# Kernel tuning notes

Measured on AMD Instinct MI355X. Metric: run time of the kernel, lower is better.

The kernel has to match this reference:

```python
import jax, jax.numpy as jnp
import numpy as np

B, S, HID = 4, 2048, 576
NH, NKV, HD = 9, 3, 64
MAXPOS, THETA = 8192, 100000.0


def rotate_half(x):
    x1, x2 = x[..., : x.shape[-1] // 2], x[..., x.shape[-1] // 2 :]
    return jnp.concatenate((-x2, x1), axis=-1)


def setup_inputs() -> dict:
    key = jax.random.key(0)
    ks = jax.random.split(key, 6)
    x = jax.random.normal(ks[0], (B, S, HID), dtype=jnp.float32)
    # RoPE tables (HuggingFace layout: freqs duplicated across halves)
    inv_freq = 1.0 / (THETA ** (np.arange(0, HD, 2, dtype=np.float32) / HD))
    freqs = np.outer(np.arange(MAXPOS, dtype=np.float32), inv_freq)
    emb = np.concatenate([freqs, freqs], axis=-1)
    cos = jnp.asarray(np.cos(emb))
    sin = jnp.asarray(np.sin(emb))
    position_ids = jnp.broadcast_to(jnp.arange(S, dtype=jnp.int64), (B, S))
    # additive causal mask [B,1,S,S]
    causal = jnp.where(
        jnp.tril(jnp.ones((S, S), dtype=bool)), 0.0, -1e9
    ).astype(jnp.float32)
    attention_mask = jnp.broadcast_to(causal, (B, 1, S, S))
    scale = 0.02
    wq = jax.random.normal(ks[1], (NH * HD, HID), dtype=jnp.float32) * scale
    wk = jax.random.normal(ks[2], (NKV * HD, HID), dtype=jnp.float32) * scale
    wv = jax.random.normal(ks[3], (NKV * HD, HID), dtype=jnp.float32) * scale
    wo = jax.random.normal(ks[4], (HID, NH * HD), dtype=jnp.float32) * scale
    return {
        "x": x, "cos": cos, "sin": sin, "position_ids": position_ids,
        "attention_mask": attention_mask,
        "wq": wq, "wk": wk, "wv": wv, "wo": wo,
    }


def reference(x, cos, sin, position_ids, attention_mask, wq, wk, wv, wo):
    b, s, _ = x.shape
    # projections (nn.Linear: y = x @ W.T), split into heads -> [B,H,S,D]
    q = (x @ wq.T).reshape(b, s, NH, HD).transpose(0, 2, 1, 3)
    k = (x @ wk.T).reshape(b, s, NKV, HD).transpose(0, 2, 1, 3)
    v = (x @ wv.T).reshape(b, s, NKV, HD).transpose(0, 2, 1, 3)
    # RoPE: cos/sin gathered per position -> [B,1,S,D], broadcast over heads
    c = cos[position_ids][:, None, :, :]
    si = sin[position_ids][:, None, :, :]
    q = q * c + rotate_half(q) * si
    k = k * c + rotate_half(k) * si
    # GQA expansion: repeat_interleave kv heads to match q heads
    k = jnp.repeat(k, NH // NKV, axis=1)
    v = jnp.repeat(v, NH // NKV, axis=1)
    scale = 1.0 / jnp.sqrt(jnp.asarray(HD, dtype=x.dtype))
    scores = jnp.einsum("bhqd,bhkd->bhqk", q, k) * scale + attention_mask
    attn = jax.nn.softmax(scores.astype(jnp.float32), axis=-1).astype(q.dtype)
    out = jnp.einsum("bhqk,bhkd->bhqd", attn, v)
    out = out.transpose(0, 2, 1, 3).reshape(b, s, NH * HD)
    return out @ wo.T
```

## Files before the change

### kernel.cpp

```cpp
#include <hip/hip_runtime.h>
#include <hip/hip_bf16.h>

#define B_    4
#define S_    2048
#define HID_  576
#define NH_   9
#define NKV_  3
#define HD_   64
#define GQ_   3

typedef __attribute__((ext_vector_type(8))) short bf16x8;
typedef __attribute__((ext_vector_type(4))) float f32x4;
typedef __attribute__((ext_vector_type(16))) float f32x16;

__device__ __forceinline__ short f2bf(float f) {
    union { float f; unsigned int u; } v; v.f = f;
    unsigned int r = (v.u + 0x7fffu + ((v.u >> 16) & 1u)) >> 16;
    return (short)r;
}

__device__ __forceinline__ unsigned int cvt_pk_bf16(float a, float b) {
    unsigned int r;
    asm("v_cvt_pk_bf16_f32 %0, %1, %2" : "=v"(r) : "v"(a), "v"(b));
    return r;
}

__device__ __forceinline__ float exp2fast(float x) {
    return __builtin_amdgcn_exp2f(x);
}

__device__ __forceinline__ void async16(const void* g, void* l) {
    __builtin_amdgcn_global_load_lds(
        (const __attribute__((address_space(1))) unsigned int*)g,
        (__attribute__((address_space(3))) unsigned int*)l, 16, 0, 0);
}

#define NX_   (8192 * 576)
#define NWQ_  (576 * 576)
#define NWK_  (192 * 576)
#define NWV_  (192 * 576)
#define NWO_  (576 * 576)
#define NTOT_ (NX_ + NWQ_ + NWK_ + NWV_ + NWO_)

__global__ __launch_bounds__(256) void convert_kernel(
    const float* __restrict__ x,  const float* __restrict__ wq,
    const float* __restrict__ wk, const float* __restrict__ wv,
    const float* __restrict__ wo,
    short* __restrict__ xb, short* __restrict__ wqkvb, short* __restrict__ wob)
{
    int i4 = (blockIdx.x * 256 + threadIdx.x) * 4;
    const float* src; short* dst;
    if (i4 < NX_)                          { src = x  + i4;                          dst = xb    + i4; }
    else if (i4 < NX_ + NWQ_)              { src = wq + (i4 - NX_);                  dst = wqkvb + (i4 - NX_); }
    else if (i4 < NX_ + NWQ_ + NWK_)       { src = wk + (i4 - NX_ - NWQ_);           dst = wqkvb + (i4 - NX_); }
    else if (i4 < NX_ + NWQ_ + NWK_ + NWV_){ src = wv + (i4 - NX_ - NWQ_ - NWK_);    dst = wqkvb + (i4 - NX_); }
    else                                   { src = wo + (i4 - NX_ - NWQ_ - NWK_ - NWV_);
                                             dst = wob + (i4 - NX_ - NWQ_ - NWK_ - NWV_); }
    float4 v = *(const float4*)src;
    short4 o = make_short4(f2bf(v.x), f2bf(v.y), f2bf(v.z), f2bf(v.w));
    *(short4*)dst = o;
}

__global__ __launch_bounds__(256) void qkv_kernel(
    const short* __restrict__ xb,
    const short* __restrict__ wqkvb,
    const float* __restrict__ cosb,
    const float* __restrict__ sinb,
    short* __restrict__ Q,
    short* __restrict__ K,
    short* __restrict__ Vt)
{
    __shared__ __align__(16) short As[2][256 * 64];
    __shared__ __align__(16) short Bs[2][64 * 64];

    const int bid = blockIdx.x;
    const int f   = (bid & 7) * 60 + (bid >> 3);
    const int m0     = (f / 15) * 256;
    const int nb_blk = f % 15;
    const int tid  = threadIdx.x;
    const int w    = tid >> 6, lane = tid & 63;
    const int quad = lane >> 4, c = lane & 15;
    const int lr   = lane >> 3, lg = lane & 7;
    const int sw   = lg ^ lr;
    const int xg   = quad ^ (c & 7);

    auto stage = [&](int step, short* dstA, short* dstB) {
        const int k0 = step * 64;
        #pragma unroll
        for (int r = 0; r < 8; ++r) {
            int ch = w * 8 + r, R = ch * 8 + lr;
            async16(xb + (size_t)(m0 + R) * HID_ + k0 + sw * 8, (char*)dstA + ch * 1024);
        }
        #pragma unroll
        for (int r = 0; r < 2; ++r) {
            int ch = w * 2 + r, R = ch * 8 + lr;
            async16(wqkvb + (size_t)(nb_blk * 64 + R) * HID_ + k0 + sw * 8, (char*)dstB + ch * 1024);
        }
    };

    f32x4 acc[4][4];
    #pragma unroll
    for (int mt = 0; mt < 4; ++mt)
        #pragma unroll
        for (int nb = 0; nb < 4; ++nb) acc[mt][nb] = (f32x4){0.f, 0.f, 0.f, 0.f};

    stage(0, As[0], Bs[0]);

    int buf = 0;
    for (int kk = 0; kk < 9; ++kk) {
        __syncthreads();
        if (kk < 8) stage(kk + 1, As[buf ^ 1], Bs[buf ^ 1]);

        const short* a_s = As[buf];
        const short* b_s = Bs[buf];
        bf16x8 bfr[4][2];
        #pragma unroll
        for (int nb = 0; nb < 4; ++nb) {
            int row = nb * 16 + c;
            bfr[nb][0] = *(const bf16x8*)(b_s + row * 64 + xg * 8);
            bfr[nb][1] = *(const bf16x8*)(b_s + row * 64 + (xg ^ 4) * 8);
        }
        #pragma unroll
        for (int mt = 0; mt < 4; ++mt) {
            int row = w * 64 + mt * 16 + c;
            bf16x8 a0 = *(const bf16x8*)(a_s + row * 64 + xg * 8);
            bf16x8 a1 = *(const bf16x8*)(a_s + row * 64 + (xg ^ 4) * 8);
            #pragma unroll
            for (int nb = 0; nb < 4; ++nb) {
                acc[mt][nb] = __builtin_amdgcn_mfma_f32_16x16x32_bf16(a0, bfr[nb][0], acc[mt][nb], 0, 0, 0);
                acc[mt][nb] = __builtin_amdgcn_mfma_f32_16x16x32_bf16(a1, bfr[nb][1], acc[mt][nb], 0, 0, 0);
            }
        }
        buf ^= 1;
    }

    int type, head;
    if (nb_blk < NH_)            { type = 0; head = nb_blk; }
    else if (nb_blk < NH_ + NKV_){ type = 1; head = nb_blk - NH_; }
    else                         { type = 2; head = nb_blk - NH_ - NKV_; }
    const int b  = m0 >> 11;
    const int s0 = m0 & (S_ - 1);

    if (type < 2) {
        const float qs = (type == 0) ? 0.18033688f : 1.0f;
        #pragma unroll
        for (int mt = 0; mt < 4; ++mt)
            #pragma unroll
            for (int reg = 0; reg < 4; ++reg) {
                int s = s0 + w * 64 + mt * 16 + quad * 4 + reg;
                const float* cr = cosb + (size_t)s * HD_;
                const float* sr = sinb + (size_t)s * HD_;
                float a0 = acc[mt][0][reg], a1 = acc[mt][1][reg];
                float a2 = acc[mt][2][reg], a3 = acc[mt][3][reg];
                float o0 = (a0 * cr[c]      - a2 * sr[c])      * qs;
                float o1 = (a1 * cr[c + 16] - a3 * sr[c + 16]) * qs;
                float o2 = (a2 * cr[c + 32] + a0 * sr[c + 32]) * qs;
                float o3 = (a3 * cr[c + 48] + a1 * sr[c + 48]) * qs;
                short* dst = (type == 0)
                    ? Q + (((size_t)b * NH_  + head) * S_ + s) * HD_
                    : K + (((size_t)b * NKV_ + head) * S_ + s) * HD_;
                dst[c]      = f2bf(o0);
                dst[c + 16] = f2bf(o1);
                dst[c + 32] = f2bf(o2);
                dst[c + 48] = f2bf(o3);
            }
    } else {
        short* base = Vt + (((size_t)b * NKV_ + head) * HD_) * S_;
        #pragma unroll
        for (int mt = 0; mt < 4; ++mt) {
            int s4 = s0 + w * 64 + mt * 16 + quad * 4;
            #pragma unroll
            for (int nb = 0; nb < 4; ++nb) {
                int d = nb * 16 + c;
                short4 pk = make_short4(f2bf(acc[mt][nb][0]), f2bf(acc[mt][nb][1]),
                                        f2bf(acc[mt][nb][2]), f2bf(acc[mt][nb][3]));
                *(short4*)(base + (size_t)d * S_ + s4) = pk;
            }
        }
    }
}

#define CPAD 528

__global__ __launch_bounds__(256) void attn_kernel(
    const short* __restrict__ Q,
    const short* __restrict__ K,
    const short* __restrict__ Vt,
    short* __restrict__ AOb)
{
    __shared__ __align__(16) char smem[33792];

    const int hb = blockIdx.x;
    const int h  = hb >> 2, b = hb & 3;
    const int qt = 31 - blockIdx.y;
    const int kh = h / GQ_;
    const int tid  = threadIdx.x;
    const int w    = tid >> 6, lane = tid & 63;
    const int l31  = lane & 31, hi = lane >> 5, l7 = lane & 7;
    const int lr   = lane >> 3, lg = lane & 7;
    const int sw   = lg ^ lr;
    const int qh   = w >> 1, kv = w & 1;
    const int rb   = (l31 >> 3) * CPAD + l7 * 64;

    const short* Qg = Q  + (((size_t)b * NH_  + h ) * S_ + qt * 64) * HD_;
    const short* Kg = K  + (((size_t)b * NKV_ + kh) * S_) * HD_;
    const short* Vg = Vt + (((size_t)b * NKV_ + kh) * HD_) * S_;

    bf16x8 aq[4];
    #pragma unroll
    for (int ks = 0; ks < 4; ++ks)
        aq[ks] = *(const bf16x8*)(Qg + (size_t)(qh * 32 + l31) * HD_ + (2 * ks + hi) * 8);

    const bool stK = (w < 2);
    const int  ch0 = (w & 1) * 4;
    const short* gs[4];
    #pragma unroll
    for (int r = 0; r < 4; ++r) {
        int ch = ch0 + r;
        gs[r] = stK ? Kg + (size_t)(ch * 8 + lr) * HD_ + sw * 8
                    : Vg + (size_t)(ch * 8 + lr) * S_  + sw * 8;
    }
    const int gstep = stK ? 64 * HD_ : 64;
    char* lbase = smem + (stK ? 0 : 16896);

    #pragma unroll
    for (int r = 0; r < 4; ++r)
        async16(gs[r], lbase + (ch0 + r) * 1056);

    f32x16 acc_o[2];
    #pragma unroll
    for (int dt = 0; dt < 2; ++dt)
        #pragma unroll
        for (int i = 0; i < 16; ++i) acc_o[dt][i] = 0.f;
    float acc_ls = 0.f;

    auto do_tile = [&](int buf, bool MASK) {
        if (MASK && kv > qh) return;
        const short* ksb = (const short*)(smem + buf * 8448);
        const short* vsb = (const short*)(smem + 16896 + buf * 8448);
        f32x16 z;
        #pragma unroll
        for (int i = 0; i < 16; ++i) z[i] = -4.0f;
        #pragma unroll
        for (int ks = 0; ks < 4; ++ks) {
            bf16x8 ak = *(const bf16x8*)(ksb + kv * 4 * CPAD + rb + ((2 * ks + hi) ^ l7) * 8);
            z = __builtin_amdgcn_mfma_f32_32x32x16_bf16(ak, aq[ks], z, 0, 0, 0);
        }
        float p[16];
        #pragma unroll
        for (int r = 0; r < 16; ++r) {
            float pv = exp2fast(z[r]);
            if (MASK && kv == qh && ((r & 3) + 8 * (r >> 2) + 4 * hi > l31)) pv = 0.f;
            p[r] = pv;
        }
        float lp = 0.f;
        #pragma unroll
        for (int r = 0; r < 16; ++r) lp += p[r];
        acc_ls += lp;
        #pragma unroll
        for (int k2 = 0; k2 < 2; ++k2) {
            unsigned int u0 = cvt_pk_bf16(p[k2 * 8 + 0], p[k2 * 8 + 1]);
            unsigned int u1 = cvt_pk_bf16(p[k2 * 8 + 2], p[k2 * 8 + 3]);
            unsigned int v0 = cvt_pk_bf16(p[k2 * 8 + 4], p[k2 * 8 + 5]);
            unsigned int v1 = cvt_pk_bf16(p[k2 * 8 + 6], p[k2 * 8 + 7]);
            asm("v_permlane32_swap_b32 %0, %1" : "+v"(u0), "+v"(v0));
            asm("v_permlane32_swap_b32 %0, %1" : "+v"(u1), "+v"(v1));
            union { unsigned int u[4]; bf16x8 v8; } af;
            af.u[0] = u0; af.u[1] = u1; af.u[2] = v0; af.u[3] = v1;
            #pragma unroll
            for (int dt = 0; dt < 2; ++dt) {
                bf16x8 bv = *(const bf16x8*)(vsb + dt * 4 * CPAD + rb + ((kv * 4 + k2 * 2 + hi) ^ l7) * 8);
                acc_o[dt] = __builtin_amdgcn_mfma_f32_32x32x16_bf16(af.v8, bv, acc_o[dt], 0, 0, 0);
            }
        }
    };

    __syncthreads();
    int buf = 0;
    for (int kt = 0; kt < qt; ++kt) {
        #pragma unroll
        for (int r = 0; r < 4; ++r) {
            gs[r] += gstep;
            async16(gs[r], lbase + (buf ^ 1) * 8448 + (ch0 + r) * 1056);
        }
        do_tile(buf, false);
        __syncthreads();
        buf ^= 1;
    }
    do_tile(buf, true);

    float ls2 = acc_ls + __shfl_xor(acc_ls, 32);
    float* sc  = (float*)smem;
    float* scl = (float*)(smem + 16384);
    __syncthreads();
    if (kv == 1) {
        #pragma unroll
        for (int dt = 0; dt < 2; ++dt)
            #pragma unroll
            for (int r = 0; r < 16; ++r)
                sc[qh * 2048 + (dt * 16 + r) * 64 + lane] = acc_o[dt][r];
        if (lane < 32) scl[qh * 32 + lane] = ls2;
    }
    __syncthreads();
    if (kv == 0) {
        #pragma unroll
        for (int dt = 0; dt < 2; ++dt)
            #pragma unroll
            for (int r = 0; r < 16; ++r)
                acc_o[dt][r] += sc[qh * 2048 + (dt * 16 + r) * 64 + lane];
        float lt = ls2 + scl[qh * 32 + l31];
        float linv = 1.0f / lt;
        if (lane < 32) scl[qh * 32 + lane] = linv;
        #pragma unroll
        for (int dt = 0; dt < 2; ++dt)
            #pragma unroll
            for (int r = 0; r < 16; ++r) {
                int q = (r & 3) + 8 * (r >> 2) + 4 * hi;
                int s = qt * 64 + qh * 32 + q;
                float li = scl[qh * 32 + q];
                AOb[(((size_t)b * S_ + s) * NH_ + h) * HD_ + dt * 32 + l31] =
                    f2bf(acc_o[dt][r] * li);
            }
    }
}

__global__ __launch_bounds__(256) void oproj_kernel(
    const short* __restrict__ AOb,
    const short* __restrict__ wob,
    float* __restrict__ out)
{
    __shared__ __align__(16) short As[2][256 * 64];
    __shared__ __align__(16) short Bs[2][64 * 64];

    const int bid = blockIdx.x;
    const int f   = (bid & 7) * 36 + (bid >> 3);
    const int m0 = (f / 9) * 256;
    const int n0 = (f % 9) * 64;
    const int tid  = threadIdx.x;
    const int w    = tid >> 6, lane = tid & 63;
    const int quad = lane >> 4, c = lane & 15;
    const int lr   = lane >> 3, lg = lane & 7;
    const int sw   = lg ^ lr;
    const int xg   = quad ^ (c & 7);

    auto stage = [&](int step, short* dstA, short* dstB) {
        const int k0 = step * 64;
        #pragma unroll
        for (int r = 0; r < 8; ++r) {
            int ch = w * 8 + r, R = ch * 8 + lr;
            async16(AOb + (size_t)(m0 + R) * HID_ + k0 + sw * 8, (char*)dstA + ch * 1024);
        }
        #pragma unroll
        for (int r = 0; r < 2; ++r) {
            int ch = w * 2 + r, R = ch * 8 + lr;
            async16(wob + (size_t)(n0 + R) * HID_ + k0 + sw * 8, (char*)dstB + ch * 1024);
        }
    };

    f32x4 acc[4][4];
    #pragma unroll
    for (int mt = 0; mt < 4; ++mt)
        #pragma unroll
        for (int nb = 0; nb < 4; ++nb) acc[mt][nb] = (f32x4){0.f, 0.f, 0.f, 0.f};

    stage(0, As[0], Bs[0]);

    int buf = 0;
    for (int kk = 0; kk < 9; ++kk) {
        __syncthreads();
        if (kk < 8) stage(kk + 1, As[buf ^ 1], Bs[buf ^ 1]);

        const short* a_s = As[buf];
        const short* b_s = Bs[buf];
        bf16x8 bfr[4][2];
        #pragma unroll
        for (int nb = 0; nb < 4; ++nb) {
            int row = nb * 16 + c;
            bfr[nb][0] = *(const bf16x8*)(b_s + row * 64 + xg * 8);
            bfr[nb][1] = *(const bf16x8*)(b_s + row * 64 + (xg ^ 4) * 8);
        }
        #pragma unroll
        for (int mt = 0; mt < 4; ++mt) {
            int row = w * 64 + mt * 16 + c;
            bf16x8 a0 = *(const bf16x8*)(a_s + row * 64 + xg * 8);
            bf16x8 a1 = *(const bf16x8*)(a_s + row * 64 + (xg ^ 4) * 8);
            #pragma unroll
            for (int nb = 0; nb < 4; ++nb) {
                acc[mt][nb] = __builtin_amdgcn_mfma_f32_16x16x32_bf16(a0, bfr[nb][0], acc[mt][nb], 0, 0, 0);
                acc[mt][nb] = __builtin_amdgcn_mfma_f32_16x16x32_bf16(a1, bfr[nb][1], acc[mt][nb], 0, 0, 0);
            }
        }
        buf ^= 1;
    }

    #pragma unroll
    for (int mt = 0; mt < 4; ++mt)
        #pragma unroll
        for (int reg = 0; reg < 4; ++reg) {
            int m = m0 + w * 64 + mt * 16 + quad * 4 + reg;
            float* dst = out + (size_t)m * HID_ + n0;
            #pragma unroll
            for (int nb = 0; nb < 4; ++nb)
                dst[nb * 16 + c] = acc[mt][nb][reg];
        }
}

extern "C" void kernel_launch(void* const* d_in, const int* in_sizes, int n_in,
                              void* d_out, int out_size, void* d_ws, size_t ws_size,
                              hipStream_t stream) {
    const float* x    = (const float*)d_in[0];
    const float* cosb = (const float*)d_in[1];
    const float* sinb = (const float*)d_in[2];
    const float* wq   = (const float*)d_in[5];
    const float* wk   = (const float*)d_in[6];
    const float* wv   = (const float*)d_in[7];
    const float* wo   = (const float*)d_in[8];

    short* xb    = (short*)d_ws;
    short* wqkvb = xb    + (size_t)NX_;
    short* wob   = wqkvb + (size_t)(NWQ_ + NWK_ + NWV_);
    short* Qb    = wob   + (size_t)NWO_;
    short* Kb    = Qb    + (size_t)B_ * NH_  * S_ * HD_;
    short* Vtb   = Kb    + (size_t)B_ * NKV_ * S_ * HD_;
    short* AOb   = Vtb   + (size_t)B_ * NKV_ * S_ * HD_;

    convert_kernel<<<dim3(NTOT_ / 4 / 256), dim3(256), 0, stream>>>(
        x, wq, wk, wv, wo, xb, wqkvb, wob);
    qkv_kernel<<<dim3(480), dim3(256), 0, stream>>>(
        xb, wqkvb, cosb, sinb, Qb, Kb, Vtb);
    attn_kernel<<<dim3(36, 32), dim3(256), 0, stream>>>(Qb, Kb, Vtb, AOb);
    oproj_kernel<<<dim3(288), dim3(256), 0, stream>>>(AOb, wob, (float*)d_out);
}
```

Before: 186.3 us.

## Triple-buffer K/V tiles in attention with two-deep async prefetch

Replaces the double-buffered K/V staging loop with a three-buffer ring that prefetches two tiles ahead, using explicit vmcnt waits and raw s_barrier instead of __syncthreads. The aim is to hide more global-load latency behind the MFMA work of the current tile. It raises shared memory per block from about 33KB to about 50KB, which may reduce the number of resident blocks per CU, and relies on hand-counted vmcnt values being correct.

```diff
diff --git a/kernel.cpp b/kernel.cpp
--- a/kernel.cpp
+++ b/kernel.cpp
@@ -181,6 +181,7 @@
 }
 
 #define CPAD 528
+#define TILEB 8448
 
 __global__ __launch_bounds__(256) void attn_kernel(
     const short* __restrict__ Q,
@@ -188,7 +189,7 @@
     const short* __restrict__ Vt,
     short* __restrict__ AOb)
 {
-    __shared__ __align__(16) char smem[33792];
+    __shared__ __align__(16) char smem[50688];
 
     const int hb = blockIdx.x;
     const int h  = hb >> 2, b = hb & 3;
@@ -213,19 +214,19 @@
 
     const bool stK = (w < 2);
     const int  ch0 = (w & 1) * 4;
-    const short* gs[4];
-    #pragma unroll
-    for (int r = 0; r < 4; ++r) {
-        int ch = ch0 + r;
-        gs[r] = stK ? Kg + (size_t)(ch * 8 + lr) * HD_ + sw * 8
-                    : Vg + (size_t)(ch * 8 + lr) * S_  + sw * 8;
-    }
-    const int gstep = stK ? 64 * HD_ : 64;
-    char* lbase = smem + (stK ? 0 : 16896);
-
-    #pragma unroll
-    for (int r = 0; r < 4; ++r)
-        async16(gs[r], lbase + (ch0 + r) * 1056);
+    const int  doff = stK ? 0 : TILEB;
+
+    auto stagebuf = [&](int kt, int ib) {
+        char* dst = smem + ib * (2 * TILEB) + doff;
+        #pragma unroll
+        for (int r = 0; r < 4; ++r) {
+            int ch = ch0 + r;
+            const short* src = stK
+                ? Kg + (size_t)(kt * 64 + ch * 8 + lr) * HD_ + sw * 8
+                : Vg + (size_t)(ch * 8 + lr) * S_ + kt * 64 + sw * 8;
+            async16(src, dst + ch * 1056);
+        }
+    };
 
     f32x16 acc_o[2];
     #pragma unroll
@@ -234,10 +235,10 @@
         for (int i = 0; i < 16; ++i) acc_o[dt][i] = 0.f;
     float acc_ls = 0.f;
 
-    auto do_tile = [&](int buf, bool MASK) {
+    auto do_tile = [&](int ib, bool MASK) {
         if (MASK && kv > qh) return;
-        const short* ksb = (const short*)(smem + buf * 8448);
-        const short* vsb = (const short*)(smem + 16896 + buf * 8448);
+        const short* ksb = (const short*)(smem + ib * (2 * TILEB));
+        const short* vsb = (const short*)(smem + ib * (2 * TILEB) + TILEB);
         f32x16 z;
         #pragma unroll
         for (int i = 0; i < 16; ++i) z[i] = -4.0f;
@@ -275,19 +276,27 @@
         }
     };
 
-    __syncthreads();
-    int buf = 0;
-    for (int kt = 0; kt < qt; ++kt) {
-        #pragma unroll
-        for (int r = 0; r < 4; ++r) {
-            gs[r] += gstep;
-            async16(gs[r], lbase + (buf ^ 1) * 8448 + (ch0 + r) * 1056);
-        }
-        do_tile(buf, false);
-        __syncthreads();
-        buf ^= 1;
-    }
-    do_tile(buf, true);
+    stagebuf(0, 0);
+    stagebuf(qt > 0 ? 1 : 0, 1);
+    asm volatile("s_waitcnt vmcnt(4)" ::: "memory");
+    __builtin_amdgcn_sched_barrier(0);
+    __builtin_amdgcn_s_barrier();
+
+    int cur = 0, pre = 2;
+    for (int kt = 0; kt <= qt; ++kt) {
+        const bool more = (kt + 2 <= qt);
+        if (more) stagebuf(kt + 2, pre);
+        do_tile(cur, kt == qt);
+        if (more) {
+            asm volatile("s_waitcnt vmcnt(4)" ::: "memory");
+        } else {
+            asm volatile("s_waitcnt vmcnt(0)" ::: "memory");
+        }
+        __builtin_amdgcn_sched_barrier(0);
+        __builtin_amdgcn_s_barrier();
+        cur = (cur == 2) ? 0 : cur + 1;
+        pre = (pre == 2) ? 0 : pre + 1;
+    }
 
     float ls2 = acc_ls + __shfl_xor(acc_ls, 32);
     float* sc  = (float*)smem;
```

After: 196.6 us. 1.05x slower.

## Compute softmax row sums via MFMA with ones vector and drop LDS padding

Applied to the files above, without the earlier changes.

Replaces the per-lane scalar accumulation of softmax probabilities with an extra MFMA that multiplies the bf16 probability fragment by a vector of ones, so row sums land in the same layout as the output accumulator. It also removes the padded shared-memory row stride in favour of an unpadded XOR-swizzled layout, shrinking LDS use. The intent is to cut VALU add work in the inner loop and simplify addressing. The trade-off is an extra matrix instruction per k-chunk, sums computed from bf16-rounded probabilities, and a possible change in bank conflicts with the new layout.

```diff
diff --git a/kernel.cpp b/kernel.cpp
--- a/kernel.cpp
+++ b/kernel.cpp
@@ -180,15 +180,13 @@
     }
 }
 
-#define CPAD 528
-
 __global__ __launch_bounds__(256) void attn_kernel(
     const short* __restrict__ Q,
     const short* __restrict__ K,
     const short* __restrict__ Vt,
     short* __restrict__ AOb)
 {
-    __shared__ __align__(16) char smem[33792];
+    __shared__ __align__(16) char smem[32768];
 
     const int hb = blockIdx.x;
     const int h  = hb >> 2, b = hb & 3;
@@ -200,7 +198,6 @@
     const int lr   = lane >> 3, lg = lane & 7;
     const int sw   = lg ^ lr;
     const int qh   = w >> 1, kv = w & 1;
-    const int rb   = (l31 >> 3) * CPAD + l7 * 64;
 
     const short* Qg = Q  + (((size_t)b * NH_  + h ) * S_ + qt * 64) * HD_;
     const short* Kg = K  + (((size_t)b * NKV_ + kh) * S_) * HD_;
@@ -213,6 +210,7 @@
 
     const bool stK = (w < 2);
     const int  ch0 = (w & 1) * 4;
+    const int  doff = stK ? 0 : 16384;
     const short* gs[4];
     #pragma unroll
     for (int r = 0; r < 4; ++r) {
@@ -221,29 +219,39 @@
                     : Vg + (size_t)(ch * 8 + lr) * S_  + sw * 8;
     }
     const int gstep = stK ? 64 * HD_ : 64;
-    char* lbase = smem + (stK ? 0 : 16896);
-
-    #pragma unroll
-    for (int r = 0; r < 4; ++r)
-        async16(gs[r], lbase + (ch0 + r) * 1056);
+
+    auto stagebuf = [&](int ib) {
+        char* dst = smem + doff + ib * 8192;
+        #pragma unroll
+        for (int r = 0; r < 4; ++r) {
+            async16(gs[r], dst + (ch0 + r) * 1024);
+            gs[r] += gstep;
+        }
+    };
+
+    bf16x8 ones;
+    #pragma unroll
+    for (int i = 0; i < 8; ++i) ones[i] = (short)0x3F80;
 
     f32x16 acc_o[2];
     #pragma unroll
     for (int dt = 0; dt < 2; ++dt)
         #pragma unroll
         for (int i = 0; i < 16; ++i) acc_o[dt][i] = 0.f;
-    float acc_ls = 0.f;
-
-    auto do_tile = [&](int buf, bool MASK) {
+    f32x16 acc_l;
+    #pragma unroll
+    for (int i = 0; i < 16; ++i) acc_l[i] = 0.f;
+
+    auto do_tile = [&](int ib, bool MASK) {
         if (MASK && kv > qh) return;
-        const short* ksb = (const short*)(smem + buf * 8448);
-        const short* vsb = (const short*)(smem + 16896 + buf * 8448);
+        const short* ksb = (const short*)(smem + ib * 8192);
+        const short* vsb = (const short*)(smem + 16384 + ib * 8192);
         f32x16 z;
         #pragma unroll
         for (int i = 0; i < 16; ++i) z[i] = -4.0f;
         #pragma unroll
         for (int ks = 0; ks < 4; ++ks) {
-            bf16x8 ak = *(const bf16x8*)(ksb + kv * 4 * CPAD + rb + ((2 * ks + hi) ^ l7) * 8);
+            bf16x8 ak = *(const bf16x8*)(ksb + (kv * 32 + l31) * 64 + ((2 * ks + hi) ^ l7) * 8);
             z = __builtin_amdgcn_mfma_f32_32x32x16_bf16(ak, aq[ks], z, 0, 0, 0);
         }
         float p[16];
@@ -253,10 +261,6 @@
             if (MASK && kv == qh && ((r & 3) + 8 * (r >> 2) + 4 * hi > l31)) pv = 0.f;
             p[r] = pv;
         }
-        float lp = 0.f;
-        #pragma unroll
-        for (int r = 0; r < 16; ++r) lp += p[r];
-        acc_ls += lp;
         #pragma unroll
         for (int k2 = 0; k2 < 2; ++k2) {
             unsigned int u0 = cvt_pk_bf16(p[k2 * 8 + 0], p[k2 * 8 + 1]);
@@ -269,27 +273,24 @@
             af.u[0] = u0; af.u[1] = u1; af.u[2] = v0; af.u[3] = v1;
             #pragma unroll
             for (int dt = 0; dt < 2; ++dt) {
-                bf16x8 bv = *(const bf16x8*)(vsb + dt * 4 * CPAD + rb + ((kv * 4 + k2 * 2 + hi) ^ l7) * 8);
+                bf16x8 bv = *(const bf16x8*)(vsb + (dt * 32 + l31) * 64 + ((kv * 4 + k2 * 2 + hi) ^ l7) * 8);
                 acc_o[dt] = __builtin_amdgcn_mfma_f32_32x32x16_bf16(af.v8, bv, acc_o[dt], 0, 0, 0);
             }
+            acc_l = __builtin_amdgcn_mfma_f32_32x32x16_bf16(af.v8, ones, acc_l, 0, 0, 0);
         }
     };
 
+    stagebuf(0);
     __syncthreads();
     int buf = 0;
     for (int kt = 0; kt < qt; ++kt) {
-        #pragma unroll
-        for (int r = 0; r < 4; ++r) {
-            gs[r] += gstep;
-            async16(gs[r], lbase + (buf ^ 1) * 8448 + (ch0 + r) * 1056);
-        }
+        stagebuf(buf ^ 1);
         do_tile(buf, false);
         __syncthreads();
         buf ^= 1;
     }
     do_tile(buf, true);
 
-    float ls2 = acc_ls + __shfl_xor(acc_ls, 32);
     float* sc  = (float*)smem;
     float* scl = (float*)(smem + 16384);
     __syncthreads();
@@ -299,27 +300,29 @@
             #pragma unroll
             for (int r = 0; r < 16; ++r)
                 sc[qh * 2048 + (dt * 16 + r) * 64 + lane] = acc_o[dt][r];
-        if (lane < 32) scl[qh * 32 + lane] = ls2;
+        if (l31 == 0) {
+            #pragma unroll
+            for (int r = 0; r < 16; ++r)
+                scl[qh * 32 + (r & 3) + 8 * (r >> 2) + 4 * hi] = acc_l[r];
+        }
     }
     __syncthreads();
     if (kv == 0) {
+        float linv[16];
+        #pragma unroll
+        for (int r = 0; r < 16; ++r) {
+            int q = (r & 3) + 8 * (r >> 2) + 4 * hi;
+            linv[r] = 1.0f / (acc_l[r] + scl[qh * 32 + q]);
+        }
         #pragma unroll
         for (int dt = 0; dt < 2; ++dt)
             #pragma unroll
-            for (int r = 0; r < 16; ++r)
-                acc_o[dt][r] += sc[qh * 2048 + (dt * 16 + r) * 64 + lane];
-        float lt = ls2 + scl[qh * 32 + l31];
-        float linv = 1.0f / lt;
-        if (lane < 32) scl[qh * 32 + lane] = linv;
-        #pragma unroll
-        for (int dt = 0; dt < 2; ++dt)
-            #pragma unroll
             for (int r = 0; r < 16; ++r) {
+                float o = acc_o[dt][r] + sc[qh * 2048 + (dt * 16 + r) * 64 + lane];
                 int q = (r & 3) + 8 * (r >> 2) + 4 * hi;
                 int s = qt * 64 + qh * 32 + q;
-                float li = scl[qh * 32 + q];
                 AOb[(((size_t)b * S_ + s) * NH_ + h) * HD_ + dt * 32 + l31] =
-                    f2bf(acc_o[dt][r] * li);
+                    f2bf(o * linv[r]);
             }
     }
 }
```

After: 188.2 us. No clear change (+1.0%).
